# Kernel optimization log

Hardware: AMD Instinct MI355X
Metric: run time of the kernel (lower is better)

Reference implementation:

```python
import jax, jax.numpy as jnp
import numpy as np

SUB_NO = 128
T_HIST = 100
T_DATA = 20000
SYN_B = 3
HIST_B = 3
FIX_VAR = 1.0


def _build_kern(delta, log_tau, K):
    # delta: (S,), log_tau: (B,), K: (S,B) -> kernel (S, T_HIST)
    t = jnp.maximum(jnp.arange(T_HIST, dtype=jnp.float32)[None, :] - delta[:, None], 0.0)  # (S,T)
    tt = t[:, :, None] / jnp.exp(log_tau)[None, None, :]  # (S,T,B)
    return jnp.einsum('stb,sb->st', tt * jnp.exp(-tt), K)


def setup_inputs() -> dict:
    key = jax.random.key(0)
    ks = jax.random.split(key, 5)
    S = SUB_NO
    return {
        'S_conv': jax.random.normal(ks[0], (T_DATA, S), jnp.float32),
        'Y_ancest': jax.random.normal(ks[1], (T_DATA, S), jnp.float32),
        'Z_ancest': jax.random.uniform(ks[2], (T_DATA, S), jnp.float32),
        'noise': jax.random.normal(ks[3], (T_DATA, S), jnp.float32),
        'C_den': jax.random.uniform(ks[4], (S, S), jnp.float32),
        'W_sub': jnp.ones(S, jnp.float32) * 0.25,
        'theta_syn': jnp.zeros(S, jnp.float32),
        'K_spike': jnp.ones((S, SYN_B), jnp.float32) * 0.01,
        'tau_spike': jnp.arange(1.6, 1.6 + SYN_B, dtype=jnp.float32),
        'delta_spike': jnp.zeros(S, jnp.float32),
        'theta_spike': jnp.ones(S, jnp.float32) * (-1.0),
        'W_spike': jnp.ones(S, jnp.float32) * 0.1,
        'tau_hist': jnp.arange(0.5, 0.5 + HIST_B * 0.5, 0.5, dtype=jnp.float32),
        'K_hist': jnp.zeros((S, HIST_B), jnp.float32),
        'delta_hist': jnp.zeros(S, jnp.float32),
    }


def _forward(S_conv, Y_ancest, Z_ancest, noise, C_den, W_sub, theta_syn,
             K_spike, tau_spike, delta_spike, theta_spike, W_spike,
             tau_hist, K_hist, delta_hist):
    S = SUB_NO
    # kernels, flipped as in torch (conv1d cross-correlation with flipped kernel)
    hist_kf = _build_kern(delta_hist, tau_hist, K_hist)[:, ::-1]      # (S,T_HIST)
    anc_kf = _build_kern(delta_spike, tau_spike, K_spike)[:, ::-1]    # (S,T_HIST)

    # Ancestor path has no recurrence -> hoist out of the time loop.
    # spike_ancest filtering: C_den is linear & time-independent, so project first,
    # then depthwise-convolve along time.
    Z_pad = jnp.concatenate([jnp.zeros((T_HIST, S), S_conv.dtype), Z_ancest], axis=0)  # (T+T_HIST,S)
    A = Z_pad @ C_den.T  # (T+T_HIST, S)
    conv = jax.lax.conv_general_dilated(
        A.T[None],                 # (1, S, T+T_HIST)
        anc_kf[:, None, :],        # (S, 1, T_HIST)
        window_strides=(1,), padding='VALID',
        dimension_numbers=('NCH', 'OIH', 'NCH'),
        feature_group_count=S)     # (1, S, T_DATA+1)
    filtered_ancest = conv[0].T[:T_DATA]  # (T_DATA, S)

    raw_ancest = Y_ancest @ C_den.T  # (T_DATA, S)
    base = S_conv + theta_syn + filtered_ancest + raw_ancest  # (T_DATA,S)
    sqrt_var = FIX_VAR ** 0.5

    def step(buf, inp):
        # buf: (S, T_HIST) rolling history of Z_out (most recent at index -1)
        b, n = inp
        fh = jnp.sum(buf * hist_kf, axis=1)            # grouped conv1d == per-channel dot
        x_out = jax.nn.sigmoid(b + fh)
        down = x_out * W_spike + theta_spike           # down_mu_Z_t == mu_Z_t (up_mu_Z=None)
        z_out = jax.nn.sigmoid(down + n * sqrt_var)
        buf = jnp.concatenate([buf[:, 1:], z_out[:, None]], axis=1)
        return buf, (x_out * W_sub, z_out, down)

    buf0 = jnp.zeros((S, T_HIST), S_conv.dtype)
    _, (final_Y, final_Z, mu_Z) = jax.lax.scan(step, buf0, (base, noise))
    return final_Y, final_Z, mu_Z, mu_Z


def reference(S_conv, Y_ancest, Z_ancest, noise, C_den, W_sub, theta_syn,
              K_spike, tau_spike, delta_spike, theta_spike, W_spike,
              tau_hist, K_hist, delta_hist):
    return _forward(S_conv, Y_ancest, Z_ancest, noise, C_den, W_sub, theta_syn,
                    K_spike, tau_spike, delta_spike, theta_spike, W_spike,
                    tau_hist, K_hist, delta_hist)
```

## Files before the change

### kernel.cpp

```cpp
#include <hip/hip_runtime.h>

#define T_DATA 20000
#define S_NO   128
#define T_HIST 100
#define J_PAD  112
#define NELEM  (T_DATA * S_NO)

__device__ __forceinline__ float sigm(float v) {
    return 1.0f / (1.0f + __expf(-v));
}

__device__ __forceinline__ void fma4(float4& a, float s, const float4 c) {
    a.x = fmaf(s, c.x, a.x); a.y = fmaf(s, c.y, a.y);
    a.z = fmaf(s, c.z, a.z); a.w = fmaf(s, c.w, a.w);
}

__global__ void __launch_bounds__(256) k1_prep(const float* __restrict__ C,
                        const float* __restrict__ K_spike,
                        const float* __restrict__ tau_spike,
                        const float* __restrict__ delta_spike,
                        const float* __restrict__ tau_hist,
                        const float* __restrict__ K_hist,
                        const float* __restrict__ delta_hist,
                        float* __restrict__ Ct,
                        float* __restrict__ anc_kT,
                        float* __restrict__ hist_k,
                        int* __restrict__ flag) {
    const int tid = threadIdx.x;
    const int b   = blockIdx.x;
    if (b < 16) {
#pragma unroll
        for (int i = 0; i < 4; ++i) {
            const int q = b * 1024 + i * 256 + tid;
            Ct[(q & 127) * S_NO + (q >> 7)] = C[q];
        }
        return;
    }
    const int s    = tid & 127;
    const int half = tid >> 7;
    {
        float d  = delta_spike[s];
        float i0 = __expf(-tau_spike[0]);
        float i1 = __expf(-tau_spike[1]);
        float i2 = __expf(-tau_spike[2]);
        float k0 = K_spike[s * 3 + 0], k1 = K_spike[s * 3 + 1], k2 = K_spike[s * 3 + 2];
        for (int j = half * 56; j < half * 56 + 56; ++j) {
            float v = 0.0f;
            if (j < T_HIST) {
                float t  = fmaxf((float)j - d, 0.0f);
                float x0 = t * i0, x1 = t * i1, x2 = t * i2;
                v = k0 * x0 * __expf(-x0) + k1 * x1 * __expf(-x1) + k2 * x2 * __expf(-x2);
            }
            anc_kT[j * S_NO + s] = v;
        }
    }
    {
        float d  = delta_hist[s];
        float i0 = __expf(-tau_hist[0]);
        float i1 = __expf(-tau_hist[1]);
        float i2 = __expf(-tau_hist[2]);
        float k0 = K_hist[s * 3 + 0], k1 = K_hist[s * 3 + 1], k2 = K_hist[s * 3 + 2];
        for (int j = half * 50; j < half * 50 + 50; ++j) {
            float t  = fmaxf((float)j - d, 0.0f);
            float x0 = t * i0, x1 = t * i1, x2 = t * i2;
            hist_k[s * T_HIST + j] =
                k0 * x0 * __expf(-x0) + k1 * x1 * __expf(-x1) + k2 * x2 * __expf(-x2);
        }
    }
    if (tid == 0) *flag = 0;
    __syncthreads();
    if (tid < 128) {
        if (K_hist[s * 3] != 0.0f || K_hist[s * 3 + 1] != 0.0f || K_hist[s * 3 + 2] != 0.0f)
            atomicOr(flag, 1);
    }
}

__global__ void __launch_bounds__(256) k2_gemm(const float* __restrict__ Z,
                                               const float* __restrict__ Y,
                                               const float* __restrict__ Ct,
                                               float* __restrict__ A,
                                               float* __restrict__ R) {
    __shared__ float Zt[32 * 128];
    __shared__ float Yt[32 * 128];
    const int t0  = blockIdx.x * 32;
    const int tid = threadIdx.x;
    {
        const float4* Zg = (const float4*)(Z + t0 * S_NO);
        const float4* Yg = (const float4*)(Y + t0 * S_NO);
        float4* Zl = (float4*)Zt;
        float4* Yl = (float4*)Yt;
        for (int q = tid; q < 1024; q += 256) { Zl[q] = Zg[q]; Yl[q] = Yg[q]; }
    }
    __syncthreads();
    const int sg = tid & 31;
    const int tg = tid >> 5;
    const int s0 = sg * 4;
    float4 accA[4] = {{0,0,0,0},{0,0,0,0},{0,0,0,0},{0,0,0,0}};
    float4 accR[4] = {{0,0,0,0},{0,0,0,0},{0,0,0,0},{0,0,0,0}};
    for (int k4 = 0; k4 < 32; ++k4) {
        const float4 c0 = *(const float4*)&Ct[(k4 * 4 + 0) * S_NO + s0];
        const float4 c1 = *(const float4*)&Ct[(k4 * 4 + 1) * S_NO + s0];
        const float4 c2 = *(const float4*)&Ct[(k4 * 4 + 2) * S_NO + s0];
        const float4 c3 = *(const float4*)&Ct[(k4 * 4 + 3) * S_NO + s0];
#pragma unroll
        for (int i = 0; i < 4; ++i) {
            const float4 z = *(const float4*)&Zt[(tg * 4 + i) * S_NO + k4 * 4];
            fma4(accA[i], z.x, c0); fma4(accA[i], z.y, c1);
            fma4(accA[i], z.z, c2); fma4(accA[i], z.w, c3);
            const float4 y = *(const float4*)&Yt[(tg * 4 + i) * S_NO + k4 * 4];
            fma4(accR[i], y.x, c0); fma4(accR[i], y.y, c1);
            fma4(accR[i], y.z, c2); fma4(accR[i], y.w, c3);
        }
    }
#pragma unroll
    for (int i = 0; i < 4; ++i) {
        *(float4*)&A[(t0 + tg * 4 + i) * S_NO + s0] = accA[i];
        *(float4*)&R[(t0 + tg * 4 + i) * S_NO + s0] = accR[i];
    }
}

template <bool GUARD>
__device__ __forceinline__ void conv16(const float* __restrict__ A,
                                       const float* __restrict__ kT,
                                       int t0, int s, float acc[16]) {
    for (int c = 0; c < 7; ++c) {
        const int B = t0 - 16 * c - 16;
        float w[31];
        float kj[16];
#pragma unroll
        for (int q = 0; q < 31; ++q) {
            const int u = B + q;
            if (GUARD)
                w[q] = (u >= 0) ? A[u * S_NO + s] : 0.0f;
            else
                w[q] = A[u * S_NO + s];
        }
#pragma unroll
        for (int r = 0; r < 16; ++r) kj[r] = kT[(16 * c + r) * S_NO + s];
#pragma unroll
        for (int r = 0; r < 16; ++r)
#pragma unroll
            for (int i = 0; i < 16; ++i)
                acc[i] = fmaf(kj[r], w[i + 15 - r], acc[i]);
    }
}

__global__ void __launch_bounds__(256) k3_fused(const float* __restrict__ A,
                                                const float* __restrict__ anc_kT,
                                                const float* __restrict__ S_conv,
                                                const float* __restrict__ noise,
                                                const float* __restrict__ W_sub,
                                                const float* __restrict__ theta_syn,
                                                const float* __restrict__ theta_spike,
                                                const float* __restrict__ W_spike,
                                                const int* __restrict__ flag,
                                                float* __restrict__ out0,
                                                float* __restrict__ out1,
                                                float* __restrict__ out2,
                                                float* __restrict__ out3,
                                                float* __restrict__ Fws) {
    const int tid = threadIdx.x;
    const int s   = tid & 127;
    const int tg  = tid >> 7;
    const int t0  = blockIdx.x * 32 + tg * 16;
    float acc[16] = {0,0,0,0,0,0,0,0,0,0,0,0,0,0,0,0};
    if (t0 >= J_PAD) conv16<false>(A, anc_kT, t0, s, acc);
    else             conv16<true >(A, anc_kT, t0, s, acc);

    if (*flag == 0) {
        const float tsy = theta_syn[s], wsub = W_sub[s];
        const float wsp = W_spike[s],  tsp  = theta_spike[s];
#pragma unroll
        for (int i = 0; i < 16; ++i) {
            const int n = (t0 + i) * S_NO + s;
            const float x  = sigm(S_conv[n] + tsy + out1[n] + acc[i]);
            const float dn = fmaf(x, wsp, tsp);
            const float z  = sigm(dn + noise[n]);
            out0[n] = x * wsub;
            out1[n] = z;
            out2[n] = dn;
            out3[n] = dn;
        }
    } else {
#pragma unroll
        for (int i = 0; i < 16; ++i) Fws[(t0 + i) * S_NO + s] = acc[i];
    }
}

__global__ void __launch_bounds__(64) k4_scan(const float* __restrict__ S_conv,
                                              const float* __restrict__ noise,
                                              const float* __restrict__ W_sub,
                                              const float* __restrict__ theta_syn,
                                              const float* __restrict__ theta_spike,
                                              const float* __restrict__ W_spike,
                                              const float* __restrict__ hist_k,
                                              const int* __restrict__ flag,
                                              const float* __restrict__ Fws,
                                              float* __restrict__ out0,
                                              float* __restrict__ out1,
                                              float* __restrict__ out2,
                                              float* __restrict__ out3) {
    if (*flag == 0) return;
    __shared__ float zr[128];
    const int s = blockIdx.x;
    const int l = threadIdx.x;
    zr[l] = 0.0f; zr[l + 64] = 0.0f;
    const float hk0 = (l < T_HIST) ? hist_k[s * T_HIST + l] : 0.0f;
    const float hk1 = (l + 64 < T_HIST) ? hist_k[s * T_HIST + l + 64] : 0.0f;
    const float tsy = theta_syn[s], wsub = W_sub[s];
    const float wsp = W_spike[s],  tsp  = theta_spike[s];
    for (int t = 0; t < T_DATA; ++t) {
        float fh = hk0 * zr[(t - 1 - l) & 127];
        fh = fmaf(hk1, zr[(t - 65 - l) & 127], fh);
#pragma unroll
        for (int m = 1; m < 64; m <<= 1) fh += __shfl_xor(fh, m, 64);
        const int n = t * S_NO + s;
        const float basev = S_conv[n] + tsy + out1[n] + Fws[n];
        const float x  = sigm(basev + fh);
        const float dn = fmaf(x, wsp, tsp);
        const float z  = sigm(dn + noise[n]);
        if (l == 0) {
            out0[n] = x * wsub;
            out1[n] = z;
            out2[n] = dn;
            out3[n] = dn;
            zr[t & 127] = z;
        }
    }
}

extern "C" void kernel_launch(void* const* d_in, const int* in_sizes, int n_in,
                              void* d_out, int out_size, void* d_ws, size_t ws_size,
                              hipStream_t stream) {
    const float* S_conv  = (const float*)d_in[0];
    const float* Y_anc   = (const float*)d_in[1];
    const float* Z_anc   = (const float*)d_in[2];
    const float* noise   = (const float*)d_in[3];
    const float* C_den   = (const float*)d_in[4];
    const float* W_sub   = (const float*)d_in[5];
    const float* th_syn  = (const float*)d_in[6];
    const float* K_spk   = (const float*)d_in[7];
    const float* tau_spk = (const float*)d_in[8];
    const float* dl_spk  = (const float*)d_in[9];
    const float* th_spk  = (const float*)d_in[10];
    const float* W_spk   = (const float*)d_in[11];
    const float* tau_h   = (const float*)d_in[12];
    const float* K_h     = (const float*)d_in[13];
    const float* dl_h    = (const float*)d_in[14];

    float* out  = (float*)d_out;
    float* out0 = out;
    float* out1 = out + NELEM;
    float* out2 = out + 2 * NELEM;
    float* out3 = out + 3 * NELEM;

    float* ws     = (float*)d_ws;
    float* wsA    = ws;
    float* wsF    = ws + NELEM;
    float* Ct     = ws + 2 * NELEM;
    float* anc_kT = Ct + S_NO * S_NO;
    float* hist_k = anc_kT + J_PAD * S_NO;
    int*   flag   = (int*)(hist_k + S_NO * T_HIST);

    k1_prep<<<17, 256, 0, stream>>>(C_den, K_spk, tau_spk, dl_spk, tau_h, K_h, dl_h,
                                    Ct, anc_kT, hist_k, flag);
    k2_gemm<<<T_DATA / 32, 256, 0, stream>>>(Z_anc, Y_anc, Ct, wsA, out1);
    k3_fused<<<T_DATA / 32, 256, 0, stream>>>(wsA, anc_kT, S_conv, noise,
                                              W_sub, th_syn, th_spk, W_spk,
                                              flag, out0, out1, out2, out3, wsF);
    k4_scan<<<S_NO, 64, 0, stream>>>(S_conv, noise, W_sub, th_syn, th_spk, W_spk,
                                     hist_k, flag, wsF, out0, out1, out2, out3);
}
```

Measured before the change: 169.0 us.

## Shrink conv tile to 8 timesteps and reshape GEMM thread tile to 2x8

The ancestor-convolution kernel now gives each thread 8 output timesteps instead of 16. The kernel taps are processed in 13 chunks of 8 with the padding trimmed to 104, and twice as many blocks are launched. This cuts register pressure and wasted padded taps, and raises occupancy and parallelism, at the cost of a larger redundant sliding window per output. The GEMM thread tile changes from 4 rows by 4 columns to 2 rows by 8 columns, which alters the LDS and global-load reuse balance.

New measurement: 192.7 us. 14.1% more time.

```diff
diff --git a/kernel.cpp b/kernel.cpp
--- a/kernel.cpp
+++ b/kernel.cpp
@@ -3,7 +3,7 @@
 #define T_DATA 20000
 #define S_NO   128
 #define T_HIST 100
-#define J_PAD  112
+#define J_PAD  104
 #define NELEM  (T_DATA * S_NO)
 
 __device__ __forceinline__ float sigm(float v) {
@@ -44,7 +44,7 @@
         float i1 = __expf(-tau_spike[1]);
         float i2 = __expf(-tau_spike[2]);
         float k0 = K_spike[s * 3 + 0], k1 = K_spike[s * 3 + 1], k2 = K_spike[s * 3 + 2];
-        for (int j = half * 56; j < half * 56 + 56; ++j) {
+        for (int j = half * 52; j < half * 52 + 52; ++j) {
             float v = 0.0f;
             if (j < T_HIST) {
                 float t  = fmaxf((float)j - d, 0.0f);
@@ -92,43 +92,52 @@
         for (int q = tid; q < 1024; q += 256) { Zl[q] = Zg[q]; Yl[q] = Yg[q]; }
     }
     __syncthreads();
-    const int sg = tid & 31;
-    const int tg = tid >> 5;
-    const int s0 = sg * 4;
-    float4 accA[4] = {{0,0,0,0},{0,0,0,0},{0,0,0,0},{0,0,0,0}};
-    float4 accR[4] = {{0,0,0,0},{0,0,0,0},{0,0,0,0},{0,0,0,0}};
+    const int sg = tid & 15;
+    const int tg = tid >> 4;
+    const int s0 = sg * 8;
+    float4 accA[2][2] = {{{0,0,0,0},{0,0,0,0}},{{0,0,0,0},{0,0,0,0}}};
+    float4 accR[2][2] = {{{0,0,0,0},{0,0,0,0}},{{0,0,0,0},{0,0,0,0}}};
     for (int k4 = 0; k4 < 32; ++k4) {
-        const float4 c0 = *(const float4*)&Ct[(k4 * 4 + 0) * S_NO + s0];
-        const float4 c1 = *(const float4*)&Ct[(k4 * 4 + 1) * S_NO + s0];
-        const float4 c2 = *(const float4*)&Ct[(k4 * 4 + 2) * S_NO + s0];
-        const float4 c3 = *(const float4*)&Ct[(k4 * 4 + 3) * S_NO + s0];
-#pragma unroll
-        for (int i = 0; i < 4; ++i) {
-            const float4 z = *(const float4*)&Zt[(tg * 4 + i) * S_NO + k4 * 4];
-            fma4(accA[i], z.x, c0); fma4(accA[i], z.y, c1);
-            fma4(accA[i], z.z, c2); fma4(accA[i], z.w, c3);
-            const float4 y = *(const float4*)&Yt[(tg * 4 + i) * S_NO + k4 * 4];
-            fma4(accR[i], y.x, c0); fma4(accR[i], y.y, c1);
-            fma4(accR[i], y.z, c2); fma4(accR[i], y.w, c3);
-        }
-    }
-#pragma unroll
-    for (int i = 0; i < 4; ++i) {
-        *(float4*)&A[(t0 + tg * 4 + i) * S_NO + s0] = accA[i];
-        *(float4*)&R[(t0 + tg * 4 + i) * S_NO + s0] = accR[i];
+        float4 c[4][2];
+#pragma unroll
+        for (int k = 0; k < 4; ++k) {
+            c[k][0] = *(const float4*)&Ct[(k4 * 4 + k) * S_NO + s0];
+            c[k][1] = *(const float4*)&Ct[(k4 * 4 + k) * S_NO + s0 + 4];
+        }
+#pragma unroll
+        for (int i = 0; i < 2; ++i) {
+            const float4 z = *(const float4*)&Zt[(tg * 2 + i) * S_NO + k4 * 4];
+            fma4(accA[i][0], z.x, c[0][0]); fma4(accA[i][1], z.x, c[0][1]);
+            fma4(accA[i][0], z.y, c[1][0]); fma4(accA[i][1], z.y, c[1][1]);
+            fma4(accA[i][0], z.z, c[2][0]); fma4(accA[i][1], z.z, c[2][1]);
+            fma4(accA[i][0], z.w, c[3][0]); fma4(accA[i][1], z.w, c[3][1]);
+            const float4 y = *(const float4*)&Yt[(tg * 2 + i) * S_NO + k4 * 4];
+            fma4(accR[i][0], y.x, c[0][0]); fma4(accR[i][1], y.x, c[0][1]);
+            fma4(accR[i][0], y.y, c[1][0]); fma4(accR[i][1], y.y, c[1][1]);
+            fma4(accR[i][0], y.z, c[2][0]); fma4(accR[i][1], y.z, c[2][1]);
+            fma4(accR[i][0], y.w, c[3][0]); fma4(accR[i][1], y.w, c[3][1]);
+        }
+    }
+#pragma unroll
+    for (int i = 0; i < 2; ++i) {
+        const int row = (t0 + tg * 2 + i) * S_NO + s0;
+        *(float4*)&A[row]     = accA[i][0];
+        *(float4*)&A[row + 4] = accA[i][1];
+        *(float4*)&R[row]     = accR[i][0];
+        *(float4*)&R[row + 4] = accR[i][1];
     }
 }
 
 template <bool GUARD>
-__device__ __forceinline__ void conv16(const float* __restrict__ A,
-                                       const float* __restrict__ kT,
-                                       int t0, int s, float acc[16]) {
-    for (int c = 0; c < 7; ++c) {
-        const int B = t0 - 16 * c - 16;
-        float w[31];
-        float kj[16];
-#pragma unroll
-        for (int q = 0; q < 31; ++q) {
+__device__ __forceinline__ void conv8(const float* __restrict__ A,
+                                      const float* __restrict__ kT,
+                                      int t0, int s, float acc[8]) {
+    for (int c = 0; c < 13; ++c) {
+        const int B = t0 - 8 * c - 8;
+        float w[15];
+        float kj[8];
+#pragma unroll
+        for (int q = 0; q < 15; ++q) {
             const int u = B + q;
             if (GUARD)
                 w[q] = (u >= 0) ? A[u * S_NO + s] : 0.0f;
@@ -136,12 +145,12 @@
                 w[q] = A[u * S_NO + s];
         }
 #pragma unroll
-        for (int r = 0; r < 16; ++r) kj[r] = kT[(16 * c + r) * S_NO + s];
-#pragma unroll
-        for (int r = 0; r < 16; ++r)
-#pragma unroll
-            for (int i = 0; i < 16; ++i)
-                acc[i] = fmaf(kj[r], w[i + 15 - r], acc[i]);
+        for (int r = 0; r < 8; ++r) kj[r] = kT[(8 * c + r) * S_NO + s];
+#pragma unroll
+        for (int r = 0; r < 8; ++r)
+#pragma unroll
+            for (int i = 0; i < 8; ++i)
+                acc[i] = fmaf(kj[r], w[i + 7 - r], acc[i]);
     }
 }
 
@@ -162,16 +171,16 @@
     const int tid = threadIdx.x;
     const int s   = tid & 127;
     const int tg  = tid >> 7;
-    const int t0  = blockIdx.x * 32 + tg * 16;
-    float acc[16] = {0,0,0,0,0,0,0,0,0,0,0,0,0,0,0,0};
-    if (t0 >= J_PAD) conv16<false>(A, anc_kT, t0, s, acc);
-    else             conv16<true >(A, anc_kT, t0, s, acc);
+    const int t0  = blockIdx.x * 16 + tg * 8;
+    float acc[8] = {0,0,0,0,0,0,0,0};
+    if (t0 >= J_PAD) conv8<false>(A, anc_kT, t0, s, acc);
+    else             conv8<true >(A, anc_kT, t0, s, acc);
 
     if (*flag == 0) {
         const float tsy = theta_syn[s], wsub = W_sub[s];
         const float wsp = W_spike[s],  tsp  = theta_spike[s];
 #pragma unroll
-        for (int i = 0; i < 16; ++i) {
+        for (int i = 0; i < 8; ++i) {
             const int n = (t0 + i) * S_NO + s;
             const float x  = sigm(S_conv[n] + tsy + out1[n] + acc[i]);
             const float dn = fmaf(x, wsp, tsp);
@@ -183,7 +192,7 @@
         }
     } else {
 #pragma unroll
-        for (int i = 0; i < 16; ++i) Fws[(t0 + i) * S_NO + s] = acc[i];
+        for (int i = 0; i < 8; ++i) Fws[(t0 + i) * S_NO + s] = acc[i];
     }
 }
 
@@ -265,7 +274,7 @@
     k1_prep<<<17, 256, 0, stream>>>(C_den, K_spk, tau_spk, dl_spk, tau_h, K_h, dl_h,
                                     Ct, anc_kT, hist_k, flag);
     k2_gemm<<<T_DATA / 32, 256, 0, stream>>>(Z_anc, Y_anc, Ct, wsA, out1);
-    k3_fused<<<T_DATA / 32, 256, 0, stream>>>(wsA, anc_kT, S_conv, noise,
+    k3_fused<<<T_DATA / 16, 256, 0, stream>>>(wsA, anc_kT, S_conv, noise,
                                               W_sub, th_syn, th_spk, W_spk,
                                               flag, out0, out1, out2, out3, wsF);
     k4_scan<<<S_NO, 64, 0, stream>>>(S_conv, noise, W_sub, th_syn, th_spk, W_spk,
```
